# Kernel tuning notes

Measured on AMD Instinct MI355X. Metric: run time of the kernel, lower is better.

The kernel has to match this reference:

```python
import jax, jax.numpy as jnp
import numpy as np

NUM_BITS = 4
BLOCK = 64
IN_F = 4096
OUT_F = 4096
RANK = 16


def dequantize(packed_qweight, weight_max, lookup_table):
    """Unpack sub-byte indices from uint8 bytes, lookup codebook, apply per-block absmax scale.
    packed_qweight: [n_bytes, 1] uint8; weight_max: [n_blocks]; lookup_table: [2**NUM_BITS].
    Returns dequantized weight [OUT_F, IN_F]."""
    nipb = 8 // NUM_BITS  # indices per byte
    mask = (1 << NUM_BITS) - 1
    b = packed_qweight[:, 0]
    # index i was packed at bit position i*NUM_BITS (LSB first)
    idx = jnp.stack([(b >> (i * NUM_BITS)) & mask for i in range(nipb)], axis=-1).reshape(-1)
    w = lookup_table[idx].reshape(-1, BLOCK) * weight_max[:, None]  # [n_blocks, BLOCK]
    return w.reshape(OUT_F, IN_F)


def setup_inputs() -> dict:
    key = jax.random.key(0)
    k0, k1, k2, k3, k4, k5 = jax.random.split(key, 6)
    x = jax.random.normal(k0, (4, 2048, IN_F), dtype=jnp.float32)
    packed_qweight = jax.random.randint(k1, (OUT_F * IN_F // (8 // NUM_BITS), 1), 0, 256, dtype=jnp.int32).astype(jnp.uint8)
    weight_max = jax.random.uniform(k2, (OUT_F * IN_F // BLOCK,), dtype=jnp.float32, minval=0.01, maxval=0.1)
    # uniform non-symmetric codebook: linspace(-1, 1, 2**num_bits)
    lookup_table = jnp.linspace(-1.0, 1.0, 2 ** NUM_BITS, dtype=jnp.float32)
    lora_A = jax.random.normal(k3, (RANK, IN_F), dtype=jnp.float32) * 0.02
    lora_B = jax.random.normal(k4, (OUT_F, RANK), dtype=jnp.float32) * 0.02
    bias = jax.random.normal(k5, (OUT_F,), dtype=jnp.float32) * 0.02
    return {"x": x, "packed_qweight": packed_qweight, "weight_max": weight_max,
            "lookup_table": lookup_table, "lora_A": lora_A, "lora_B": lora_B, "bias": bias}


def reference(x, packed_qweight, weight_max, lookup_table, lora_A, lora_B, bias):
    W = dequantize(packed_qweight, weight_max, lookup_table)  # [OUT_F, IN_F]
    base = jnp.einsum('bsi,oi->bso', x, W)
    lora = jnp.einsum('bsr,or->bso', jnp.einsum('bsi,ri->bsr', x, lora_A), lora_B)
    return base + lora + bias
```

## Files before the change

### kernel.cpp

```cpp
#include <hip/hip_runtime.h>
#include <hip/hip_bf16.h>
#include <stdint.h>

constexpr int IN_F  = 4096;
constexpr int OUT_F = 4096;
constexpr int M_ROWS = 4 * 2048;
constexpr int RANK = 16;

typedef short short8 __attribute__((ext_vector_type(8)));
typedef float f32x4 __attribute__((ext_vector_type(4)));

__device__ __forceinline__ short f2bf(float f) {
  return __builtin_bit_cast(short, __float2bfloat16(f));
}

__device__ __forceinline__ void gload16(const void* g, void* l) {
  __builtin_amdgcn_global_load_lds(
      (const __attribute__((address_space(1))) void*)g,
      (__attribute__((address_space(3))) void*)l, 16, 0, 0);
}

__global__ __launch_bounds__(256) void dequant_lora_kernel(
    const int* __restrict__ q,
    const float* __restrict__ wmax,
    const float* __restrict__ lut,
    const float* __restrict__ lA,
    const float* __restrict__ lB,
    __hip_bfloat16* __restrict__ W) {
  __shared__ float slut[16];
  if (threadIdx.x < 16) slut[threadIdx.x] = lut[threadIdx.x];
  __syncthreads();

  const int o0  = blockIdx.y * 64 + (threadIdx.x >> 5) * 8;
  const int ib0 = blockIdx.x * 512 + (threadIdx.x & 31) * 16;

  #pragma unroll
  for (int h = 0; h < 2; ++h) {
    const int ib = ib0 + h * 8;
    float w[8][8];
    #pragma unroll
    for (int p = 0; p < 8; ++p) {
      const size_t l = (size_t)(o0 + p) * IN_F + ib;
      const int4 u = *(const int4*)(q + (l >> 1));
      const float sc = wmax[l >> 6];
      w[p][0] = slut[u.x & 15] * sc;
      w[p][1] = slut[(u.x >> 4) & 15] * sc;
      w[p][2] = slut[u.y & 15] * sc;
      w[p][3] = slut[(u.y >> 4) & 15] * sc;
      w[p][4] = slut[u.z & 15] * sc;
      w[p][5] = slut[(u.z >> 4) & 15] * sc;
      w[p][6] = slut[u.w & 15] * sc;
      w[p][7] = slut[(u.w >> 4) & 15] * sc;
    }
    #pragma unroll 2
    for (int r = 0; r < 16; ++r) {
      const float* ar = lA + (size_t)r * IN_F + ib;
      const float4 a0 = *(const float4*)(ar);
      const float4 a1 = *(const float4*)(ar + 4);
      float b[8];
      #pragma unroll
      for (int p = 0; p < 8; ++p) b[p] = lB[(size_t)(o0 + p) * RANK + r];
      #pragma unroll
      for (int p = 0; p < 8; ++p) {
        w[p][0] += b[p] * a0.x; w[p][1] += b[p] * a0.y;
        w[p][2] += b[p] * a0.z; w[p][3] += b[p] * a0.w;
        w[p][4] += b[p] * a1.x; w[p][5] += b[p] * a1.y;
        w[p][6] += b[p] * a1.z; w[p][7] += b[p] * a1.w;
      }
    }
    #pragma unroll
    for (int p = 0; p < 8; ++p) {
      short8 s;
      #pragma unroll
      for (int qq = 0; qq < 8; ++qq) s[qq] = f2bf(w[p][qq]);
      *(short8*)&W[(size_t)(o0 + p) * IN_F + ib] = s;
    }
  }
}

__global__ __launch_bounds__(256) void cvt_x_kernel(
    const float* __restrict__ x, __hip_bfloat16* __restrict__ xb) {
  constexpr int NG = (M_ROWS * IN_F) / 8;
  const int stride = gridDim.x * blockDim.x;
  for (int i = blockIdx.x * blockDim.x + threadIdx.x; i < NG; i += stride) {
    const float4 a = ((const float4*)x)[2 * i];
    const float4 b = ((const float4*)x)[2 * i + 1];
    short8 s;
    s[0] = f2bf(a.x); s[1] = f2bf(a.y); s[2] = f2bf(a.z); s[3] = f2bf(a.w);
    s[4] = f2bf(b.x); s[5] = f2bf(b.y); s[6] = f2bf(b.z); s[7] = f2bf(b.w);
    ((short8*)xb)[i] = s;
  }
}

constexpr int BM = 256, BN = 256, BK = 64;
constexpr int GM = M_ROWS, GN = OUT_F, GK = IN_F;
constexpr int NKT = GK / BK;

#define LOAD_B(BUF, KH)                                                   \
  _Pragma("unroll")                                                       \
  for (int n_ = 0; n_ < 4; ++n_)                                          \
    bf[n_] = *(const short8*)&sB[BUF][KH][wn * 64 + n_ * 16 + lr][lk * 8];

#define LOAD_A(BUF, KH, MH)                                               \
  _Pragma("unroll")                                                       \
  for (int i_ = 0; i_ < 4; ++i_)                                          \
    af[i_] = *(const short8*)&sA[BUF][KH][wm * 128 + (MH) * 64 + i_ * 16 + lr][lk * 8];

#define MFMA_Q(MH)                                                        \
  __builtin_amdgcn_s_setprio(1);                                          \
  _Pragma("unroll")                                                       \
  for (int i_ = 0; i_ < 4; ++i_)                                          \
    _Pragma("unroll")                                                     \
    for (int n_ = 0; n_ < 4; ++n_)                                        \
      acc[(MH) * 4 + i_][n_] = __builtin_amdgcn_mfma_f32_16x16x32_bf16(   \
          af[i_], bf[n_], acc[(MH) * 4 + i_][n_], 0, 0, 0);               \
  __builtin_amdgcn_s_setprio(0);

#define PHASE(BUF, KH, MH, DOB, GB, LB, VM)                               \
  do {                                                                    \
    if (DOB) { LOAD_B(BUF, KH) }                                          \
    LOAD_A(BUF, KH, MH)                                                   \
    stage(GB, LB);                                                        \
    if (VM) asm volatile("s_waitcnt vmcnt(6)" ::: "memory");              \
    asm volatile("s_barrier" ::: "memory");                               \
    asm volatile("s_waitcnt lgkmcnt(0)" ::: "memory");                    \
    __builtin_amdgcn_sched_barrier(0);                                    \
    MFMA_Q(MH)                                                            \
    asm volatile("s_barrier" ::: "memory");                               \
  } while (0)

__global__ __launch_bounds__(512, 2) void gemm_bt_8phase(
    const __hip_bfloat16* __restrict__ A,
    const __hip_bfloat16* __restrict__ B,
    const float* __restrict__ bias,
    float* __restrict__ C) {
  __shared__ __hip_bfloat16 sA[2][2][256][32];
  __shared__ __hip_bfloat16 sB[2][2][256][32];

  const int tid  = threadIdx.x;
  const int lane = tid & 63;
  const int wave = tid >> 6;
  const int lr = lane & 15;
  const int lk = lane >> 4;
  const int wm = wave >> 2;
  const int wn = wave & 3;

  const int bid = blockIdx.x;
  const int cpx = gridDim.x >> 3;
  const int wg  = (bid & 7) * cpx + (bid >> 3);
  const int nbn = GN / BN;
  const int m0 = (wg / nbn) * BM;
  const int n0 = (wg % nbn) * BN;

  const __hip_bfloat16* Abase = A + (size_t)m0 * GK;
  const __hip_bfloat16* Bbase = B + (size_t)n0 * GK;

  auto stage = [&](const __hip_bfloat16* gb, __hip_bfloat16* lb) {
    #pragma unroll
    for (int j = 0; j < 2; ++j) {
      const int c = j * 512 + tid;
      const int row = c >> 2, slot = c & 3;
      gload16(gb + (size_t)row * GK + slot * 8,
              (void*)((char*)lb + (j * 512 + wave * 64) * 16));
    }
  };

  f32x4 acc[8][4];
  #pragma unroll
  for (int m = 0; m < 8; ++m)
    #pragma unroll
    for (int n = 0; n < 4; ++n) acc[m][n] = (f32x4)0.0f;

  stage(Abase +  0, &sA[0][0][0][0]);
  stage(Bbase +  0, &sB[0][0][0][0]);
  stage(Abase + 32, &sA[0][1][0][0]);
  stage(Bbase + 32, &sB[0][1][0][0]);
  stage(Bbase + 64, &sB[1][0][0][0]);
  stage(Abase + 64, &sA[1][0][0][0]);
  stage(Bbase + 96, &sB[1][1][0][0]);
  asm volatile("s_waitcnt vmcnt(6)" ::: "memory");
  asm volatile("s_barrier" ::: "memory");

  short8 af[4], bf[4];

  for (int t = 0; t < NKT; t += 2) {
    const int t2 = (t + 2 < NKT) ? t + 2 : NKT - 1;
    const int t3 = (t + 3 < NKT) ? t + 3 : NKT - 1;

    PHASE(0, 0, 0, true,  Abase + (size_t)(t + 1) * 64 + 32, &sA[1][1][0][0], false);
    PHASE(0, 0, 1, false, Bbase + (size_t)t2 * 64,           &sB[0][0][0][0], false);
    PHASE(0, 1, 0, true,  Abase + (size_t)t2 * 64,           &sA[0][0][0][0], false);
    PHASE(0, 1, 1, false, Bbase + (size_t)t2 * 64 + 32,      &sB[0][1][0][0], true);
    PHASE(1, 0, 0, true,  Abase + (size_t)t2 * 64 + 32,      &sA[0][1][0][0], false);
    PHASE(1, 0, 1, false, Bbase + (size_t)t3 * 64,           &sB[1][0][0][0], false);
    PHASE(1, 1, 0, true,  Abase + (size_t)t3 * 64,           &sA[1][0][0][0], false);
    PHASE(1, 1, 1, false, Bbase + (size_t)t3 * 64 + 32,      &sB[1][1][0][0], true);
  }

  #pragma unroll
  for (int n = 0; n < 4; ++n) {
    const int col = n0 + wn * 64 + n * 16 + lr;
    const float bv = bias[col];
    #pragma unroll
    for (int m = 0; m < 8; ++m) {
      const int row = m0 + wm * 128 + m * 16 + lk * 4;
      #pragma unroll
      for (int j = 0; j < 4; ++j)
        C[(size_t)(row + j) * GN + col] = acc[m][n][j] + bv;
    }
  }
}

extern "C" void kernel_launch(void* const* d_in, const int* in_sizes, int n_in,
                              void* d_out, int out_size, void* d_ws, size_t ws_size,
                              hipStream_t stream) {
  const float* x    = (const float*)d_in[0];
  const int*   qw   = (const int*)d_in[1];
  const float* wmax = (const float*)d_in[2];
  const float* lut  = (const float*)d_in[3];
  const float* lA   = (const float*)d_in[4];
  const float* lB   = (const float*)d_in[5];
  const float* bias = (const float*)d_in[6];
  float* out = (float*)d_out;

  __hip_bfloat16* Weff = (__hip_bfloat16*)d_ws;
  __hip_bfloat16* xb   = (__hip_bfloat16*)((char*)d_ws + (size_t)OUT_F * IN_F * 2);

  dequant_lora_kernel<<<dim3(IN_F / 512, OUT_F / 64), 256, 0, stream>>>(
      qw, wmax, lut, lA, lB, Weff);
  cvt_x_kernel<<<2048, 256, 0, stream>>>(x, xb);
  gemm_bt_8phase<<<(GM / BM) * (GN / BN), 512, 0, stream>>>(xb, Weff, bias, out);
}
```

Before: 336.2 us.

## Double-buffer LDS fragments in registers and XOR-swizzle LDS layout in GEMM

The GEMM main loop now keeps two register sets of A/B fragments, so each phase prefetches the next phase's fragments from LDS while the current MFMAs run. The lgkmcnt wait is relaxed to a nonzero count to allow that overlap. The global-to-LDS staging and the fragment reads also apply a matching XOR swizzle on the 16-byte k-slot, meant to reduce LDS bank conflicts. This raises register pressure and adds fragile waitcnt and index logic that must stay consistent with the swizzle.

```diff
diff --git a/kernel.cpp b/kernel.cpp
--- a/kernel.cpp
+++ b/kernel.cpp
@@ -96,36 +96,42 @@
 constexpr int GM = M_ROWS, GN = OUT_F, GK = IN_F;
 constexpr int NKT = GK / BK;
 
-#define LOAD_B(BUF, KH)                                                   \
+#define LOAD_Bn(RB_, RKH, DST)                                            \
   _Pragma("unroll")                                                       \
   for (int n_ = 0; n_ < 4; ++n_)                                          \
-    bf[n_] = *(const short8*)&sB[BUF][KH][wn * 64 + n_ * 16 + lr][lk * 8];
-
-#define LOAD_A(BUF, KH, MH)                                               \
+    bfr[DST][n_] = *(const short8*)&sB[RB_][RKH][wn * 64 + n_ * 16 + lr][swr * 8];
+
+#define LOAD_An(RB_, RKH, RMH, DST)                                       \
   _Pragma("unroll")                                                       \
   for (int i_ = 0; i_ < 4; ++i_)                                          \
-    af[i_] = *(const short8*)&sA[BUF][KH][wm * 128 + (MH) * 64 + i_ * 16 + lr][lk * 8];
-
-#define MFMA_Q(MH)                                                        \
+    afr[DST][i_] = *(const short8*)&sA[RB_][RKH][wm * 128 + (RMH) * 64 + i_ * 16 + lr][swr * 8];
+
+#define MFMA_Q(CMH, AC, BC)                                               \
   __builtin_amdgcn_s_setprio(1);                                          \
   _Pragma("unroll")                                                       \
   for (int i_ = 0; i_ < 4; ++i_)                                          \
     _Pragma("unroll")                                                     \
     for (int n_ = 0; n_ < 4; ++n_)                                        \
-      acc[(MH) * 4 + i_][n_] = __builtin_amdgcn_mfma_f32_16x16x32_bf16(   \
-          af[i_], bf[n_], acc[(MH) * 4 + i_][n_], 0, 0, 0);               \
+      acc[(CMH) * 4 + i_][n_] = __builtin_amdgcn_mfma_f32_16x16x32_bf16(  \
+          afr[AC][i_], bfr[BC][n_], acc[(CMH) * 4 + i_][n_], 0, 0, 0);    \
   __builtin_amdgcn_s_setprio(0);
 
-#define PHASE(BUF, KH, MH, DOB, GB, LB, VM)                               \
+#define PHASE(AC, BC, DOB, RBUF, RKH, RMH, CMH, GB, LB, VM, NLG)          \
   do {                                                                    \
-    if (DOB) { LOAD_B(BUF, KH) }                                          \
-    LOAD_A(BUF, KH, MH)                                                   \
-    stage(GB, LB);                                                        \
-    if (VM) asm volatile("s_waitcnt vmcnt(6)" ::: "memory");              \
+    if (VM) {                                                             \
+      stage(GB, LB);                                                      \
+      asm volatile("s_waitcnt vmcnt(6)" ::: "memory");                    \
+      if (DOB) { LOAD_Bn(RBUF, RKH, (BC) ^ 1) }                           \
+      LOAD_An(RBUF, RKH, RMH, (AC) ^ 1)                                   \
+    } else {                                                              \
+      if (DOB) { LOAD_Bn(RBUF, RKH, (BC) ^ 1) }                           \
+      LOAD_An(RBUF, RKH, RMH, (AC) ^ 1)                                   \
+      stage(GB, LB);                                                      \
+    }                                                                     \
     asm volatile("s_barrier" ::: "memory");                               \
-    asm volatile("s_waitcnt lgkmcnt(0)" ::: "memory");                    \
+    asm volatile("s_waitcnt lgkmcnt(" #NLG ")" ::: "memory");             \
     __builtin_amdgcn_sched_barrier(0);                                    \
-    MFMA_Q(MH)                                                            \
+    MFMA_Q(CMH, AC, BC)                                                   \
     asm volatile("s_barrier" ::: "memory");                               \
   } while (0)
 
@@ -144,6 +150,7 @@
   const int lk = lane >> 4;
   const int wm = wave >> 2;
   const int wn = wave & 3;
+  const int swr = lk ^ ((lr >> 1) & 3);
 
   const int bid = blockIdx.x;
   const int cpx = gridDim.x >> 3;
@@ -155,12 +162,14 @@
   const __hip_bfloat16* Abase = A + (size_t)m0 * GK;
   const __hip_bfloat16* Bbase = B + (size_t)n0 * GK;
 
+  const int swst = (tid >> 3) & 3;
   auto stage = [&](const __hip_bfloat16* gb, __hip_bfloat16* lb) {
     #pragma unroll
     for (int j = 0; j < 2; ++j) {
       const int c = j * 512 + tid;
       const int row = c >> 2, slot = c & 3;
-      gload16(gb + (size_t)row * GK + slot * 8,
+      const int sg = slot ^ swst;
+      gload16(gb + (size_t)row * GK + sg * 8,
               (void*)((char*)lb + (j * 512 + wave * 64) * 16));
     }
   };
@@ -181,20 +190,22 @@
   asm volatile("s_waitcnt vmcnt(6)" ::: "memory");
   asm volatile("s_barrier" ::: "memory");
 
-  short8 af[4], bf[4];
+  short8 afr[2][4], bfr[2][4];
+  LOAD_Bn(0, 0, 0)
+  LOAD_An(0, 0, 0, 0)
 
   for (int t = 0; t < NKT; t += 2) {
     const int t2 = (t + 2 < NKT) ? t + 2 : NKT - 1;
     const int t3 = (t + 3 < NKT) ? t + 3 : NKT - 1;
 
-    PHASE(0, 0, 0, true,  Abase + (size_t)(t + 1) * 64 + 32, &sA[1][1][0][0], false);
-    PHASE(0, 0, 1, false, Bbase + (size_t)t2 * 64,           &sB[0][0][0][0], false);
-    PHASE(0, 1, 0, true,  Abase + (size_t)t2 * 64,           &sA[0][0][0][0], false);
-    PHASE(0, 1, 1, false, Bbase + (size_t)t2 * 64 + 32,      &sB[0][1][0][0], true);
-    PHASE(1, 0, 0, true,  Abase + (size_t)t2 * 64 + 32,      &sA[0][1][0][0], false);
-    PHASE(1, 0, 1, false, Bbase + (size_t)t3 * 64,           &sB[1][0][0][0], false);
-    PHASE(1, 1, 0, true,  Abase + (size_t)t3 * 64,           &sA[1][0][0][0], false);
-    PHASE(1, 1, 1, false, Bbase + (size_t)t3 * 64 + 32,      &sB[1][1][0][0], true);
+    PHASE(0, 0, 0,  0, 0, 1, 0,  Abase + (size_t)(t + 1) * 64 + 32, &sA[1][1][0][0], 0, 4);
+    PHASE(1, 0, 1,  0, 1, 0, 1,  Bbase + (size_t)t2 * 64,           &sB[0][0][0][0], 0, 8);
+    PHASE(0, 1, 0,  0, 1, 1, 0,  Abase + (size_t)t2 * 64,           &sA[0][0][0][0], 0, 4);
+    PHASE(1, 1, 1,  1, 0, 0, 1,  Bbase + (size_t)t2 * 64 + 32,      &sB[0][1][0][0], 1, 8);
+    PHASE(0, 0, 0,  1, 0, 1, 0,  Abase + (size_t)t2 * 64 + 32,      &sA[0][1][0][0], 0, 4);
+    PHASE(1, 0, 1,  1, 1, 0, 1,  Bbase + (size_t)t3 * 64,           &sB[1][0][0][0], 0, 8);
+    PHASE(0, 1, 0,  1, 1, 1, 0,  Abase + (size_t)t3 * 64,           &sA[1][0][0][0], 0, 4);
+    PHASE(1, 1, 1,  0, 0, 0, 1,  Bbase + (size_t)t3 * 64 + 32,      &sB[1][1][0][0], 1, 8);
   }
 
   #pragma unroll
```

Result: no change. 341.7 us (+1.7%).
